# Kernel tuning notes

Hardware: AMD Instinct MI355X
Metric: run time of the kernel (lower is better)

## Reference

```python
import jax, jax.numpy as jnp
import numpy as np

N_NODES = 50000
N_EDGES = 1600000
D = 128
NUM_GRAPHS = 64


def gcn_conv(x, src, dst, ew, W, b, n):
    # PyG GCNConv: add self-loops (weight 1), symmetric normalization,
    # message = norm * (x @ W)[src], aggregated at dst, then + bias.
    loop = jnp.arange(n)
    src2 = jnp.concatenate([src, loop])
    dst2 = jnp.concatenate([dst, loop])
    ew2 = jnp.concatenate([ew, jnp.ones((n,), dtype=x.dtype)])
    deg = jax.ops.segment_sum(ew2, dst2, num_segments=n)  # [N]
    dinv = jnp.where(deg > 0, jax.lax.rsqrt(deg), 0.0)
    norm = dinv[src2] * ew2 * dinv[dst2]                  # [E+N]
    xw = x @ W                                            # [N, out]
    msg = xw[src2] * norm[:, None]                        # [E+N, out]
    return jax.ops.segment_sum(msg, dst2, num_segments=n) + b


def setup_inputs() -> dict:
    key = jax.random.key(0)
    ks = jax.random.split(key, 10)
    x = jax.random.normal(ks[0], (N_NODES, D), dtype=jnp.float32)
    edge_index = jax.random.randint(ks[1], (2, N_EDGES), 0, N_NODES, dtype=jnp.int32)
    edge_weight = jax.random.uniform(ks[2], (N_EDGES,), dtype=jnp.float32)
    batch = jnp.sort(jax.random.randint(ks[3], (N_NODES,), 0, NUM_GRAPHS, dtype=jnp.int32))
    s = 1.0 / np.sqrt(D)
    W0 = jax.random.uniform(ks[4], (D, D), jnp.float32, -s, s)
    W1 = jax.random.uniform(ks[5], (D, D), jnp.float32, -s, s)
    W2 = jax.random.uniform(ks[6], (D, D), jnp.float32, -s, s)
    b0 = jnp.zeros((D,), jnp.float32)
    b1 = jnp.zeros((D,), jnp.float32)
    b2 = jnp.zeros((D,), jnp.float32)
    return {"x": x, "edge_index": edge_index, "edge_weight": edge_weight,
            "batch": batch, "W0": W0, "b0": b0, "W1": W1, "b1": b1,
            "W2": W2, "b2": b2}


def reference(x, edge_index, edge_weight, batch, W0, b0, W1, b1, W2, b2):
    src, dst = edge_index[0], edge_index[1]
    n = x.shape[0]
    h = gcn_conv(x, src, dst, edge_weight, W0, b0, n)
    h = jax.nn.relu(h)  # dropout=0.0 (eval)
    h = gcn_conv(h, src, dst, edge_weight, W1, b1, n)
    h = jax.nn.relu(h)
    h = gcn_conv(h, src, dst, edge_weight, W2, b2, n)
    # global mean pool over graphs in the batch
    sums = jax.ops.segment_sum(h, batch, num_segments=NUM_GRAPHS)
    cnts = jax.ops.segment_sum(jnp.ones((n,), h.dtype), batch, num_segments=NUM_GRAPHS)
    return sums / jnp.maximum(cnts, 1.0)[:, None]
```

## Files before the change

kernel.cpp:

```cpp
#include <hip/hip_runtime.h>
#include <hip/hip_fp16.h>


#define DFEAT 128
#define BLK_E 4096

typedef _Float16 half8 __attribute__((ext_vector_type(8)));
typedef float floatx4 __attribute__((ext_vector_type(4)));

__device__ __forceinline__ int wave_incl_scan(int v) {
    int incl = v;
    #pragma unroll
    for (int off = 1; off < 64; off <<= 1) {
        int u = __shfl_up(incl, (unsigned)off, 64);
        if ((int)(threadIdx.x & 63) >= off) incl += u;
    }
    return incl;
}

__global__ __launch_bounds__(256) void hist_k(const int* __restrict__ dst,
                                              int* __restrict__ hist,
                                              int E, int nblk, int nbuck) {
    __shared__ int h[256];
    int tid = threadIdx.x, b = blockIdx.x;
    h[tid] = 0;
    __syncthreads();
    int base = b * BLK_E;
    int nE = min(BLK_E, E - base);
    for (int i = tid; i < nE; i += 256) atomicAdd(&h[dst[base + i] >> 8], 1);
    __syncthreads();
    if (tid < nbuck) hist[tid * nblk + b] = h[tid];
}

__global__ __launch_bounds__(256) void scanb_k(int* __restrict__ arr,
                                               int* __restrict__ blksum,
                                               int n_val, int n_scan) {
    int tid = threadIdx.x;
    int base = blockIdx.x * 1024 + tid * 4;
    int v0 = (base + 0 < n_val) ? arr[base + 0] : 0;
    int v1 = (base + 1 < n_val) ? arr[base + 1] : 0;
    int v2 = (base + 2 < n_val) ? arr[base + 2] : 0;
    int v3 = (base + 3 < n_val) ? arr[base + 3] : 0;
    int tsum = v0 + v1 + v2 + v3;
    int incl = wave_incl_scan(tsum);
    __shared__ int wtot[4];
    if ((tid & 63) == 63) wtot[tid >> 6] = incl;
    __syncthreads();
    int woff = 0;
    for (int w = 0; w < (tid >> 6); w++) woff += wtot[w];
    int texcl = woff + incl - tsum;
    if (base + 0 < n_scan) arr[base + 0] = texcl;
    if (base + 1 < n_scan) arr[base + 1] = texcl + v0;
    if (base + 2 < n_scan) arr[base + 2] = texcl + v0 + v1;
    if (base + 3 < n_scan) arr[base + 3] = texcl + v0 + v1 + v2;
    if (tid == 255) blksum[blockIdx.x] = woff + incl;
}

__global__ __launch_bounds__(256) void scan_small256(int* __restrict__ blksum, int nb) {
    int tid = threadIdx.x;
    int v = (tid < nb) ? blksum[tid] : 0;
    int incl = wave_incl_scan(v);
    __shared__ int wtot[4];
    if ((tid & 63) == 63) wtot[tid >> 6] = incl;
    __syncthreads();
    int woff = 0;
    for (int w = 0; w < (tid >> 6); w++) woff += wtot[w];
    if (tid < nb) blksum[tid] = woff + incl - v;
}

__global__ void scanf_k(int* __restrict__ arr, const int* __restrict__ blksum, int n_scan) {
    int i = blockIdx.x * 256 + threadIdx.x;
    if (i < n_scan) arr[i] += blksum[i >> 10];
}

__global__ __launch_bounds__(256) void scat_k(const int* __restrict__ src,
                                              const int* __restrict__ dst,
                                              const float* __restrict__ ew,
                                              const int* __restrict__ offs,
                                              uint2* __restrict__ rec,
                                              int E, int nblk, int nbuck) {
    __shared__ int lcur[256];
    __shared__ int gbase[256];
    __shared__ uint2 srec[BLK_E];
    __shared__ int gpos[BLK_E];
    int tid = threadIdx.x, b = blockIdx.x;
    lcur[tid] = 0;
    __syncthreads();
    int base = b * BLK_E;
    int nE = min(BLK_E, E - base);
    for (int i = tid; i < nE; i += 256) atomicAdd(&lcur[dst[base + i] >> 8], 1);
    __syncthreads();
    int v = lcur[tid];
    int incl = wave_incl_scan(v);
    __shared__ int wtot[4];
    if ((tid & 63) == 63) wtot[tid >> 6] = incl;
    __syncthreads();
    int woff = 0;
    for (int w = 0; w < (tid >> 6); w++) woff += wtot[w];
    int excl = woff + incl - v;
    __syncthreads();
    lcur[tid] = excl;
    gbase[tid] = (tid < nbuck) ? (offs[tid * nblk + b] - excl) : 0;
    __syncthreads();
    for (int i = tid; i < nE; i += 256) {
        int e = base + i;
        int d = dst[e];
        int bin = d >> 8;
        int slot = atomicAdd(&lcur[bin], 1);
        uint2 r;
        r.x = (unsigned)src[e] | ((unsigned)(d & 255) << 16);
        r.y = __float_as_uint(ew[e]);
        srec[slot] = r;
        gpos[slot] = gbase[bin] + slot;
    }
    __syncthreads();
    for (int i = tid; i < nE; i += 256) rec[gpos[i]] = srec[i];
}

__global__ __launch_bounds__(1024) void bucket_k(const uint2* __restrict__ rec,
                                                 const int* __restrict__ offs,
                                                 float* __restrict__ dinv,
                                                 int* __restrict__ row_ptr,
                                                 uint2* __restrict__ csr,
                                                 int N, int nblk) {
    __shared__ int cnt[256];
    __shared__ unsigned degfx[256];
    __shared__ int excl_s[256];
    __shared__ int cur[256];
    __shared__ int wtot[4];
    int tid = threadIdx.x, bin = blockIdx.x;
    int start = offs[bin * nblk];
    int endp = offs[(bin + 1) * nblk];
    if (tid < 256) { cnt[tid] = 0; degfx[tid] = 0; }
    __syncthreads();
    for (int i = start + tid; i < endp; i += 1024) {
        uint2 r = rec[i];
        int dl = (r.x >> 16) & 255;
        atomicAdd(&cnt[dl], 1);
        atomicAdd(&degfx[dl], (unsigned)(__uint_as_float(r.y) * 1048576.0f + 0.5f));
    }
    __syncthreads();
    int v = 0, incl = 0;
    if (tid < 256) { v = cnt[tid]; incl = wave_incl_scan(v); }
    if (tid < 256 && (tid & 63) == 63) wtot[tid >> 6] = incl;
    __syncthreads();
    if (tid < 256) {
        int woff = 0;
        for (int w = 0; w < (tid >> 6); w++) woff += wtot[w];
        int e = woff + incl - v;
        excl_s[tid] = e;
        cur[tid] = e;
        int node = bin * 256 + tid;
        if (node < N) {
            row_ptr[node] = start + e;
            float deg = (float)degfx[tid] * (1.0f / 1048576.0f) + 1.0f;
            float di = rsqrtf(deg);
            dinv[node] = di;
            degfx[tid] = __float_as_uint(di);
        }
    }
    __syncthreads();
    for (int i = start + tid; i < endp; i += 1024) {
        uint2 r = rec[i];
        int dl = (r.x >> 16) & 255;
        int p = start + atomicAdd(&cur[dl], 1);
        float di_d = __uint_as_float(degfx[dl]);
        uint2 c;
        c.x = r.x & 0xffff;
        c.y = __float_as_uint(__uint_as_float(r.y) * di_d);
        csr[p] = c;
    }
}

__global__ void normfix_k(uint2* __restrict__ csr, const float* __restrict__ dinv,
                          int* __restrict__ row_ptr, int E, int N) {
    int e = blockIdx.x * 256 + threadIdx.x;
    if (e < E) {
        uint2 c = csr[e];
        c.y = __float_as_uint(__uint_as_float(c.y) * dinv[c.x]);
        csr[e] = c;
    }
    if (e == 0) row_ptr[N] = E;
}

__global__ void wconv_k(const float* __restrict__ W0, const float* __restrict__ W1,
                        const float* __restrict__ W2, _Float16* __restrict__ Wsw) {
    int idx = blockIdx.x * 256 + threadIdx.x;
    if (idx >= 3 * 128 * 128) return;
    int w = idx >> 14;
    int r = idx & 16383;
    int k = r >> 7, nn = r & 127;
    const float* W = (w == 0) ? W0 : (w == 1) ? W1 : W2;
    float v = W[k * 128 + nn];
    _Float16 hi = (_Float16)v;
    _Float16 lo = (_Float16)((v - (float)hi) * 1024.0f);
    int kk = k >> 5, quad = (k >> 3) & 3, j = k & 7;
    int t = nn >> 4, L = quad * 16 + (nn & 15);
    int off = ((kk * 8 + t) * 64 + L) * 8 + j;
    Wsw[(size_t)(w * 2 + 0) * 16384 + off] = hi;
    Wsw[(size_t)(w * 2 + 1) * 16384 + off] = lo;
}

__global__ __launch_bounds__(256) void gemm_mfma(const _Float16* __restrict__ A,
                                                 const _Float16* __restrict__ Wsw,
                                                 _Float16* __restrict__ C, int n) {
    __shared__ _Float16 Bl[2 * 16384];
    {
        const uint4* s = (const uint4*)Wsw;
        uint4* d = (uint4*)Bl;
        for (int i = threadIdx.x; i < 4096; i += 256) d[i] = s[i];
    }
    int wave = threadIdx.x >> 6, lane = threadIdx.x & 63;
    int quad = lane >> 4, mcol = lane & 15;
    int row0 = blockIdx.x * 64 + wave * 16 + mcol;
    half8 af[4] = {};
    if (row0 < n) {
        const half8* Arow = (const half8*)(A + (size_t)row0 * DFEAT);
        af[0] = Arow[0 + quad];
        af[1] = Arow[4 + quad];
        af[2] = Arow[8 + quad];
        af[3] = Arow[12 + quad];
    }
    __syncthreads();
    floatx4 acch[8] = {};
    floatx4 accl[8] = {};
    const half8* Bh = (const half8*)Bl;
    const half8* Blo = (const half8*)(Bl + 16384);
    #pragma unroll
    for (int kk = 0; kk < 4; kk++) {
        #pragma unroll
        for (int t = 0; t < 8; t++) {
            half8 bh = Bh[(kk * 8 + t) * 64 + lane];
            acch[t] = __builtin_amdgcn_mfma_f32_16x16x32_f16(af[kk], bh, acch[t], 0, 0, 0);
            half8 bl = Blo[(kk * 8 + t) * 64 + lane];
            accl[t] = __builtin_amdgcn_mfma_f32_16x16x32_f16(af[kk], bl, accl[t], 0, 0, 0);
        }
    }
    int orow_base = blockIdx.x * 64 + wave * 16 + quad * 4;
    #pragma unroll
    for (int t = 0; t < 8; t++) {
        #pragma unroll
        for (int r = 0; r < 4; r++) {
            int orow = orow_base + r;
            if (orow < n) {
                float v = acch[t][r] + accl[t][r] * (1.0f / 1024.0f);
                C[(size_t)orow * DFEAT + t * 16 + mcol] = (_Float16)v;
            }
        }
    }
}

__global__ __launch_bounds__(256) void gemm_mfma_f32(const float* __restrict__ A,
                                                     const _Float16* __restrict__ Wsw,
                                                     _Float16* __restrict__ C, int n) {
    __shared__ _Float16 Bl[2 * 16384];
    {
        const uint4* s = (const uint4*)Wsw;
        uint4* d = (uint4*)Bl;
        for (int i = threadIdx.x; i < 4096; i += 256) d[i] = s[i];
    }
    int wave = threadIdx.x >> 6, lane = threadIdx.x & 63;
    int quad = lane >> 4, mcol = lane & 15;
    int row0 = blockIdx.x * 64 + wave * 16 + mcol;
    half8 af[4] = {};
    if (row0 < n) {
        const float4* Arow = (const float4*)(A + (size_t)row0 * DFEAT);
        #pragma unroll
        for (int kk = 0; kk < 4; kk++) {
            float4 f0 = Arow[kk * 8 + quad * 2];
            float4 f1 = Arow[kk * 8 + quad * 2 + 1];
            half8 a;
            a[0] = (_Float16)f0.x; a[1] = (_Float16)f0.y;
            a[2] = (_Float16)f0.z; a[3] = (_Float16)f0.w;
            a[4] = (_Float16)f1.x; a[5] = (_Float16)f1.y;
            a[6] = (_Float16)f1.z; a[7] = (_Float16)f1.w;
            af[kk] = a;
        }
    }
    __syncthreads();
    floatx4 acch[8] = {};
    floatx4 accl[8] = {};
    const half8* Bh = (const half8*)Bl;
    const half8* Blo = (const half8*)(Bl + 16384);
    #pragma unroll
    for (int kk = 0; kk < 4; kk++) {
        #pragma unroll
        for (int t = 0; t < 8; t++) {
            half8 bh = Bh[(kk * 8 + t) * 64 + lane];
            acch[t] = __builtin_amdgcn_mfma_f32_16x16x32_f16(af[kk], bh, acch[t], 0, 0, 0);
            half8 bl = Blo[(kk * 8 + t) * 64 + lane];
            accl[t] = __builtin_amdgcn_mfma_f32_16x16x32_f16(af[kk], bl, accl[t], 0, 0, 0);
        }
    }
    int orow_base = blockIdx.x * 64 + wave * 16 + quad * 4;
    #pragma unroll
    for (int t = 0; t < 8; t++) {
        #pragma unroll
        for (int r = 0; r < 4; r++) {
            int orow = orow_base + r;
            if (orow < n) {
                float v = acch[t][r] + accl[t][r] * (1.0f / 1024.0f);
                C[(size_t)orow * DFEAT + t * 16 + mcol] = (_Float16)v;
            }
        }
    }
}

__global__ __launch_bounds__(256) void agg_k(const __half2* __restrict__ xw2,
                                             const int* __restrict__ row_ptr,
                                             const int2* __restrict__ csr,
                                             const float* __restrict__ dinv,
                                             const float* __restrict__ bias,
                                             __half2* __restrict__ out, int relu, int n) {
    int node = blockIdx.x * 4 + (threadIdx.x >> 6);
    if (node >= n) return;
    int lane = threadIdx.x & 63;
    float di = dinv[node];
    float2 selfv = __half22float2(xw2[(size_t)node * 64 + lane]);
    float sc = di * di;
    float ax = sc * selfv.x, ay = sc * selfv.y;
    int e = row_ptr[node], end = row_ptr[node + 1];
    for (; e + 8 <= end; e += 8) {
        int2 c0 = csr[e + 0], c1 = csr[e + 1], c2 = csr[e + 2], c3 = csr[e + 3];
        int2 c4 = csr[e + 4], c5 = csr[e + 5], c6 = csr[e + 6], c7 = csr[e + 7];
        float2 v0 = __half22float2(xw2[(size_t)c0.x * 64 + lane]);
        float2 v1 = __half22float2(xw2[(size_t)c1.x * 64 + lane]);
        float2 v2 = __half22float2(xw2[(size_t)c2.x * 64 + lane]);
        float2 v3 = __half22float2(xw2[(size_t)c3.x * 64 + lane]);
        float2 v4 = __half22float2(xw2[(size_t)c4.x * 64 + lane]);
        float2 v5 = __half22float2(xw2[(size_t)c5.x * 64 + lane]);
        float2 v6 = __half22float2(xw2[(size_t)c6.x * 64 + lane]);
        float2 v7 = __half22float2(xw2[(size_t)c7.x * 64 + lane]);
        float w0 = __int_as_float(c0.y), w1 = __int_as_float(c1.y);
        float w2 = __int_as_float(c2.y), w3 = __int_as_float(c3.y);
        float w4 = __int_as_float(c4.y), w5 = __int_as_float(c5.y);
        float w6 = __int_as_float(c6.y), w7 = __int_as_float(c7.y);
        ax = fmaf(w0, v0.x, ax); ay = fmaf(w0, v0.y, ay);
        ax = fmaf(w1, v1.x, ax); ay = fmaf(w1, v1.y, ay);
        ax = fmaf(w2, v2.x, ax); ay = fmaf(w2, v2.y, ay);
        ax = fmaf(w3, v3.x, ax); ay = fmaf(w3, v3.y, ay);
        ax = fmaf(w4, v4.x, ax); ay = fmaf(w4, v4.y, ay);
        ax = fmaf(w5, v5.x, ax); ay = fmaf(w5, v5.y, ay);
        ax = fmaf(w6, v6.x, ax); ay = fmaf(w6, v6.y, ay);
        ax = fmaf(w7, v7.x, ax); ay = fmaf(w7, v7.y, ay);
    }
    for (; e < end; e++) {
        int2 c = csr[e];
        float w = __int_as_float(c.y);
        float2 v = __half22float2(xw2[(size_t)c.x * 64 + lane]);
        ax = fmaf(w, v.x, ax); ay = fmaf(w, v.y, ay);
    }
    float2 bv = ((const float2*)bias)[lane];
    ax += bv.x; ay += bv.y;
    if (relu) { ax = fmaxf(ax, 0.f); ay = fmaxf(ay, 0.f); }
    out[(size_t)node * 64 + lane] = __floats2half2_rn(ax, ay);
}

__global__ __launch_bounds__(128) void pool_k(const __half* __restrict__ h,
                                              const int* __restrict__ batch,
                                              float* __restrict__ out,
                                              float* __restrict__ pool_cnt, int n) {
    int j = threadIdx.x;
    int start = blockIdx.x * 64;
    if (start >= n) return;
    int end = start + 64; if (end > n) end = n;
    int g = batch[start];
    float acc = 0.f;
    float ccnt = 0.f;
    for (int i = start; i < end; i++) {
        int bi = batch[i];
        if (bi != g) {
            atomicAdd(&out[g * DFEAT + j], acc);
            if (j == 0) atomicAdd(&pool_cnt[g], ccnt);
            acc = 0.f; ccnt = 0.f; g = bi;
        }
        acc += __half2float(h[(size_t)i * DFEAT + j]);
        ccnt += 1.f;
    }
    atomicAdd(&out[g * DFEAT + j], acc);
    if (j == 0) atomicAdd(&pool_cnt[g], ccnt);
}

__global__ void div_k(float* __restrict__ out, const float* __restrict__ cnt) {
    int idx = blockIdx.x * 256 + threadIdx.x;
    if (idx < 64 * DFEAT) {
        float c = cnt[idx >> 7];
        out[idx] = out[idx] / fmaxf(c, 1.0f);
    }
}

extern "C" void kernel_launch(void* const* d_in, const int* in_sizes, int n_in,
                              void* d_out, int out_size, void* d_ws, size_t ws_size,
                              hipStream_t stream) {
    const float* x    = (const float*)d_in[0];
    const int*  eidx  = (const int*)d_in[1];
    const float* ew   = (const float*)d_in[2];
    const int*  batch = (const int*)d_in[3];
    const float* W0 = (const float*)d_in[4];
    const float* b0 = (const float*)d_in[5];
    const float* W1 = (const float*)d_in[6];
    const float* b1 = (const float*)d_in[7];
    const float* W2 = (const float*)d_in[8];
    const float* b2 = (const float*)d_in[9];
    float* out = (float*)d_out;

    const int N = in_sizes[0] / DFEAT;
    const int E = in_sizes[2];
    const int* src = eidx;
    const int* dst = eidx + E;

    const int nbuck = (N + 255) / 256;
    const int nblk  = (E + BLK_E - 1) / BLK_E;
    const int total = nbuck * nblk;
    const int n_scan = total + 1;

    size_t off = 0;
    auto walloc = [&](size_t bytes) -> void* {
        void* p = (char*)d_ws + off;
        off += (bytes + 255) & ~(size_t)255;
        return p;
    };
    float*   dinv    = (float*)  walloc((size_t)N * 4);
    int*     row_ptr = (int*)    walloc((size_t)(N + 1) * 4);
    int*     offs    = (int*)    walloc((size_t)n_scan * 4);
    int*     blksum  = (int*)    walloc(256 * 4);
    uint2*   rec     = (uint2*)  walloc((size_t)E * 8);
    uint2*   csr     = (uint2*)  walloc((size_t)E * 8);
    _Float16* xwH    = (_Float16*)walloc((size_t)N * DFEAT * 2);
    _Float16* hH     = (_Float16*)walloc((size_t)N * DFEAT * 2);
    _Float16* Wsw    = (_Float16*)walloc((size_t)6 * 16384 * 2);
    float*   pool_cnt= (float*)  walloc(64 * 4);

    hipMemsetAsync(out, 0, (size_t)64 * DFEAT * 4, stream);
    hipMemsetAsync(pool_cnt, 0, 64 * 4, stream);

    hist_k<<<nblk, 256, 0, stream>>>(dst, offs, E, nblk, nbuck);
    int nsb = (n_scan + 1023) / 1024;
    scanb_k<<<nsb, 256, 0, stream>>>(offs, blksum, total, n_scan);
    scan_small256<<<1, 256, 0, stream>>>(blksum, nsb);
    scanf_k<<<(n_scan + 255) / 256, 256, 0, stream>>>(offs, blksum, n_scan);
    scat_k<<<nblk, 256, 0, stream>>>(src, dst, ew, offs, rec, E, nblk, nbuck);
    bucket_k<<<nbuck, 1024, 0, stream>>>(rec, offs, dinv, row_ptr, csr, N, nblk);
    normfix_k<<<(E + 255) / 256, 256, 0, stream>>>(csr, dinv, row_ptr, E, N);

    wconv_k<<<(3 * 16384 + 255) / 256, 256, 0, stream>>>(W0, W1, W2, Wsw);

    int gG = (N + 63) / 64;
    int gA = (N + 3) / 4;
    gemm_mfma_f32<<<gG, 256, 0, stream>>>(x, Wsw + (size_t)0 * 32768, xwH, N);
    agg_k<<<gA, 256, 0, stream>>>((const __half2*)xwH, row_ptr, (const int2*)csr,
                                  dinv, b0, (__half2*)hH, 1, N);
    gemm_mfma<<<gG, 256, 0, stream>>>(hH, Wsw + (size_t)1 * 32768, xwH, N);
    agg_k<<<gA, 256, 0, stream>>>((const __half2*)xwH, row_ptr, (const int2*)csr,
                                  dinv, b1, (__half2*)hH, 1, N);
    gemm_mfma<<<gG, 256, 0, stream>>>(hH, Wsw + (size_t)2 * 32768, xwH, N);
    agg_k<<<gA, 256, 0, stream>>>((const __half2*)xwH, row_ptr, (const int2*)csr,
                                  dinv, b2, (__half2*)hH, 0, N);

    pool_k<<<(N + 63) / 64, 128, 0, stream>>>((const __half*)hH, batch, out, pool_cnt, N);
    div_k<<<32, 256, 0, stream>>>(out, pool_cnt);
}
```

Before: 399.8 us.

## Fold scan fixup into consumers, sort CSR by source partition, widen agg loads

Removes the scanf_k pass by having scat_k and bucket_k add the block-scan offset when they read offs. bucket_k now orders each node's edges into four source-index partitions, so gathers within a row follow a roughly ascending source order and should hit cache better. agg_k splits each wave into two halves that each handle alternate edges with 8-byte loads of four features, then combines the halves with a cross-lane shuffle. This roughly halves the gather instructions per edge, but half the lanes sit idle at the store and odd-length tails need masked padding loads.

```diff
diff --git a/kernel.cpp b/kernel.cpp
--- a/kernel.cpp
+++ b/kernel.cpp
@@ -68,15 +68,11 @@
     if (tid < nb) blksum[tid] = woff + incl - v;
 }
 
-__global__ void scanf_k(int* __restrict__ arr, const int* __restrict__ blksum, int n_scan) {
-    int i = blockIdx.x * 256 + threadIdx.x;
-    if (i < n_scan) arr[i] += blksum[i >> 10];
-}
-
 __global__ __launch_bounds__(256) void scat_k(const int* __restrict__ src,
                                               const int* __restrict__ dst,
                                               const float* __restrict__ ew,
                                               const int* __restrict__ offs,
+                                              const int* __restrict__ blksum,
                                               uint2* __restrict__ rec,
                                               int E, int nblk, int nbuck) {
     __shared__ int lcur[256];
@@ -100,7 +96,8 @@
     int excl = woff + incl - v;
     __syncthreads();
     lcur[tid] = excl;
-    gbase[tid] = (tid < nbuck) ? (offs[tid * nblk + b] - excl) : 0;
+    int oidx = tid * nblk + b;
+    gbase[tid] = (tid < nbuck) ? (offs[oidx] + blksum[oidx >> 10] - excl) : 0;
     __syncthreads();
     for (int i = tid; i < nE; i += 256) {
         int e = base + i;
@@ -119,40 +116,42 @@
 
 __global__ __launch_bounds__(1024) void bucket_k(const uint2* __restrict__ rec,
                                                  const int* __restrict__ offs,
+                                                 const int* __restrict__ blksum,
                                                  float* __restrict__ dinv,
                                                  int* __restrict__ row_ptr,
                                                  uint2* __restrict__ csr,
                                                  int N, int nblk) {
-    __shared__ int cnt[256];
+    __shared__ int cnt[1024];
     __shared__ unsigned degfx[256];
-    __shared__ int excl_s[256];
-    __shared__ int cur[256];
-    __shared__ int wtot[4];
+    __shared__ int cur[1024];
+    __shared__ int wtot[16];
     int tid = threadIdx.x, bin = blockIdx.x;
-    int start = offs[bin * nblk];
-    int endp = offs[(bin + 1) * nblk];
-    if (tid < 256) { cnt[tid] = 0; degfx[tid] = 0; }
+    int idx0 = bin * nblk, idx1 = (bin + 1) * nblk;
+    int start = offs[idx0] + blksum[idx0 >> 10];
+    int endp  = offs[idx1] + blksum[idx1 >> 10];
+    cnt[tid] = 0;
+    if (tid < 256) degfx[tid] = 0;
     __syncthreads();
     for (int i = start + tid; i < endp; i += 1024) {
         uint2 r = rec[i];
         int dl = (r.x >> 16) & 255;
-        atomicAdd(&cnt[dl], 1);
+        int part = (r.x & 0xffff) >> 14;
+        atomicAdd(&cnt[dl * 4 + part], 1);
         atomicAdd(&degfx[dl], (unsigned)(__uint_as_float(r.y) * 1048576.0f + 0.5f));
     }
     __syncthreads();
-    int v = 0, incl = 0;
-    if (tid < 256) { v = cnt[tid]; incl = wave_incl_scan(v); }
-    if (tid < 256 && (tid & 63) == 63) wtot[tid >> 6] = incl;
+    int v = cnt[tid];
+    int incl = wave_incl_scan(v);
+    if ((tid & 63) == 63) wtot[tid >> 6] = incl;
+    __syncthreads();
+    int woff = 0;
+    for (int w = 0; w < (tid >> 6); w++) woff += wtot[w];
+    cur[tid] = woff + incl - v;
     __syncthreads();
     if (tid < 256) {
-        int woff = 0;
-        for (int w = 0; w < (tid >> 6); w++) woff += wtot[w];
-        int e = woff + incl - v;
-        excl_s[tid] = e;
-        cur[tid] = e;
         int node = bin * 256 + tid;
         if (node < N) {
-            row_ptr[node] = start + e;
+            row_ptr[node] = start + cur[tid * 4];
             float deg = (float)degfx[tid] * (1.0f / 1048576.0f) + 1.0f;
             float di = rsqrtf(deg);
             dinv[node] = di;
@@ -163,10 +162,12 @@
     for (int i = start + tid; i < endp; i += 1024) {
         uint2 r = rec[i];
         int dl = (r.x >> 16) & 255;
-        int p = start + atomicAdd(&cur[dl], 1);
+        int s = r.x & 0xffff;
+        int part = s >> 14;
+        int p = start + atomicAdd(&cur[dl * 4 + part], 1);
         float di_d = __uint_as_float(degfx[dl]);
         uint2 c;
-        c.x = r.x & 0xffff;
+        c.x = (unsigned)s;
         c.y = __float_as_uint(__uint_as_float(r.y) * di_d);
         csr[p] = c;
     }
@@ -306,54 +307,72 @@
     }
 }
 
-__global__ __launch_bounds__(256) void agg_k(const __half2* __restrict__ xw2,
+__global__ __launch_bounds__(256) void agg_k(const _Float16* __restrict__ xw,
                                              const int* __restrict__ row_ptr,
                                              const int2* __restrict__ csr,
                                              const float* __restrict__ dinv,
                                              const float* __restrict__ bias,
-                                             __half2* __restrict__ out, int relu, int n) {
+                                             _Float16* __restrict__ out, int relu, int n) {
     int node = blockIdx.x * 4 + (threadIdx.x >> 6);
     if (node >= n) return;
     int lane = threadIdx.x & 63;
-    float di = dinv[node];
-    float2 selfv = __half22float2(xw2[(size_t)node * 64 + lane]);
-    float sc = di * di;
-    float ax = sc * selfv.x, ay = sc * selfv.y;
+    int hf = lane >> 5;
+    int fl = lane & 31;
+    const _Float16* base = xw + fl * 4;
+    float a0 = 0.f, a1 = 0.f, a2 = 0.f, a3 = 0.f;
+    {
+        float di = dinv[node];
+        float sw = (hf == 0) ? di * di : 0.f;
+        uint2 r = *(const uint2*)(base + (size_t)node * DFEAT);
+        float2 f0 = __half22float2(*(__half2*)&r.x);
+        float2 f1 = __half22float2(*(__half2*)&r.y);
+        a0 = sw * f0.x; a1 = sw * f0.y; a2 = sw * f1.x; a3 = sw * f1.y;
+    }
     int e = row_ptr[node], end = row_ptr[node + 1];
     for (; e + 8 <= end; e += 8) {
-        int2 c0 = csr[e + 0], c1 = csr[e + 1], c2 = csr[e + 2], c3 = csr[e + 3];
-        int2 c4 = csr[e + 4], c5 = csr[e + 5], c6 = csr[e + 6], c7 = csr[e + 7];
-        float2 v0 = __half22float2(xw2[(size_t)c0.x * 64 + lane]);
-        float2 v1 = __half22float2(xw2[(size_t)c1.x * 64 + lane]);
-        float2 v2 = __half22float2(xw2[(size_t)c2.x * 64 + lane]);
-        float2 v3 = __half22float2(xw2[(size_t)c3.x * 64 + lane]);
-        float2 v4 = __half22float2(xw2[(size_t)c4.x * 64 + lane]);
-        float2 v5 = __half22float2(xw2[(size_t)c5.x * 64 + lane]);
-        float2 v6 = __half22float2(xw2[(size_t)c6.x * 64 + lane]);
-        float2 v7 = __half22float2(xw2[(size_t)c7.x * 64 + lane]);
+        int2 c0 = csr[e + 0 + hf];
+        int2 c1 = csr[e + 2 + hf];
+        int2 c2 = csr[e + 4 + hf];
+        int2 c3 = csr[e + 6 + hf];
+        uint2 r0 = *(const uint2*)(base + (size_t)c0.x * DFEAT);
+        uint2 r1 = *(const uint2*)(base + (size_t)c1.x * DFEAT);
+        uint2 r2 = *(const uint2*)(base + (size_t)c2.x * DFEAT);
+        uint2 r3 = *(const uint2*)(base + (size_t)c3.x * DFEAT);
         float w0 = __int_as_float(c0.y), w1 = __int_as_float(c1.y);
         float w2 = __int_as_float(c2.y), w3 = __int_as_float(c3.y);
-        float w4 = __int_as_float(c4.y), w5 = __int_as_float(c5.y);
-        float w6 = __int_as_float(c6.y), w7 = __int_as_float(c7.y);
-        ax = fmaf(w0, v0.x, ax); ay = fmaf(w0, v0.y, ay);
-        ax = fmaf(w1, v1.x, ax); ay = fmaf(w1, v1.y, ay);
-        ax = fmaf(w2, v2.x, ax); ay = fmaf(w2, v2.y, ay);
-        ax = fmaf(w3, v3.x, ax); ay = fmaf(w3, v3.y, ay);
-        ax = fmaf(w4, v4.x, ax); ay = fmaf(w4, v4.y, ay);
-        ax = fmaf(w5, v5.x, ax); ay = fmaf(w5, v5.y, ay);
-        ax = fmaf(w6, v6.x, ax); ay = fmaf(w6, v6.y, ay);
-        ax = fmaf(w7, v7.x, ax); ay = fmaf(w7, v7.y, ay);
-    }
-    for (; e < end; e++) {
-        int2 c = csr[e];
-        float w = __int_as_float(c.y);
-        float2 v = __half22float2(xw2[(size_t)c.x * 64 + lane]);
-        ax = fmaf(w, v.x, ax); ay = fmaf(w, v.y, ay);
-    }
-    float2 bv = ((const float2*)bias)[lane];
-    ax += bv.x; ay += bv.y;
-    if (relu) { ax = fmaxf(ax, 0.f); ay = fmaxf(ay, 0.f); }
-    out[(size_t)node * 64 + lane] = __floats2half2_rn(ax, ay);
+        #define ACC(R, W)                                              \
+        {                                                              \
+            float2 f0 = __half22float2(*(__half2*)&R.x);               \
+            float2 f1 = __half22float2(*(__half2*)&R.y);               \
+            a0 = fmaf(W, f0.x, a0); a1 = fmaf(W, f0.y, a1);            \
+            a2 = fmaf(W, f1.x, a2); a3 = fmaf(W, f1.y, a3);            \
+        }
+        ACC(r0, w0) ACC(r1, w1) ACC(r2, w2) ACC(r3, w3)
+    }
+    for (; e < end; e += 2) {
+        int ee = e + hf;
+        int s = 0; float w = 0.f;
+        if (ee < end) { int2 c = csr[ee]; s = c.x; w = __int_as_float(c.y); }
+        uint2 r = *(const uint2*)(base + (size_t)s * DFEAT);
+        ACC(r, w)
+    }
+    #undef ACC
+    a0 += __shfl_xor(a0, 32, 64);
+    a1 += __shfl_xor(a1, 32, 64);
+    a2 += __shfl_xor(a2, 32, 64);
+    a3 += __shfl_xor(a3, 32, 64);
+    if (hf == 0) {
+        float4 bv = *(const float4*)(bias + fl * 4);
+        a0 += bv.x; a1 += bv.y; a2 += bv.z; a3 += bv.w;
+        if (relu) {
+            a0 = fmaxf(a0, 0.f); a1 = fmaxf(a1, 0.f);
+            a2 = fmaxf(a2, 0.f); a3 = fmaxf(a3, 0.f);
+        }
+        __half2 o0 = __floats2half2_rn(a0, a1);
+        __half2 o1 = __floats2half2_rn(a2, a3);
+        uint2 st; st.x = *(unsigned*)&o0; st.y = *(unsigned*)&o1;
+        *(uint2*)(out + (size_t)node * DFEAT + fl * 4) = st;
+    }
 }
 
 __global__ __launch_bounds__(128) void pool_k(const __half* __restrict__ h,
@@ -438,9 +457,8 @@
     int nsb = (n_scan + 1023) / 1024;
     scanb_k<<<nsb, 256, 0, stream>>>(offs, blksum, total, n_scan);
     scan_small256<<<1, 256, 0, stream>>>(blksum, nsb);
-    scanf_k<<<(n_scan + 255) / 256, 256, 0, stream>>>(offs, blksum, n_scan);
-    scat_k<<<nblk, 256, 0, stream>>>(src, dst, ew, offs, rec, E, nblk, nbuck);
-    bucket_k<<<nbuck, 1024, 0, stream>>>(rec, offs, dinv, row_ptr, csr, N, nblk);
+    scat_k<<<nblk, 256, 0, stream>>>(src, dst, ew, offs, blksum, rec, E, nblk, nbuck);
+    bucket_k<<<nbuck, 1024, 0, stream>>>(rec, offs, blksum, dinv, row_ptr, csr, N, nblk);
     normfix_k<<<(E + 255) / 256, 256, 0, stream>>>(csr, dinv, row_ptr, E, N);
 
     wconv_k<<<(3 * 16384 + 255) / 256, 256, 0, stream>>>(W0, W1, W2, Wsw);
@@ -448,14 +466,11 @@
     int gG = (N + 63) / 64;
     int gA = (N + 3) / 4;
     gemm_mfma_f32<<<gG, 256, 0, stream>>>(x, Wsw + (size_t)0 * 32768, xwH, N);
-    agg_k<<<gA, 256, 0, stream>>>((const __half2*)xwH, row_ptr, (const int2*)csr,
-                                  dinv, b0, (__half2*)hH, 1, N);
+    agg_k<<<gA, 256, 0, stream>>>(xwH, row_ptr, (const int2*)csr, dinv, b0, hH, 1, N);
     gemm_mfma<<<gG, 256, 0, stream>>>(hH, Wsw + (size_t)1 * 32768, xwH, N);
-    agg_k<<<gA, 256, 0, stream>>>((const __half2*)xwH, row_ptr, (const int2*)csr,
-                                  dinv, b1, (__half2*)hH, 1, N);
+    agg_k<<<gA, 256, 0, stream>>>(xwH, row_ptr, (const int2*)csr, dinv, b1, hH, 1, N);
     gemm_mfma<<<gG, 256, 0, stream>>>(hH, Wsw + (size_t)2 * 32768, xwH, N);
-    agg_k<<<gA, 256, 0, stream>>>((const __half2*)xwH, row_ptr, (const int2*)csr,
-                                  dinv, b2, (__half2*)hH, 0, N);
+    agg_k<<<gA, 256, 0, stream>>>(xwH, row_ptr, (const int2*)csr, dinv, b2, hH, 0, N);
 
     pool_k<<<(N + 63) / 64, 128, 0, stream>>>((const __half*)hH, batch, out, pool_cnt, N);
     div_k<<<32, 256, 0, stream>>>(out, pool_cnt);
```

Measured after the change: 399.4 us. Within noise of the previous version (-0.1%).
